# Optimization experiments

Measured on AMD Instinct MI355X. Metric: run time of the kernel, lower is better.

The kernel has to match this reference:

```python
import jax, jax.numpy as jnp
import numpy as np

N, E, IN_F, H, F = 4096, 131072, 512, 8, 32  # n_nodes, n_edges, in_features, n_heads, n_hidden
SLOPE = 0.2


def setup_inputs() -> dict:
    key = jax.random.key(0)
    k1, k2, k3, k4 = jax.random.split(key, 4)
    h = jax.random.normal(k1, (N, IN_F), dtype=jnp.float32)
    edge_index = jax.random.randint(k2, (2, E), 0, N)
    train_mask = jnp.ones((E + N,), dtype=jnp.float32)  # mask values written into adj (incl. self-loops appended in forward)
    W_fc = jax.random.normal(k3, (IN_F, H * F), dtype=jnp.float32) * (1.0 / np.sqrt(IN_F))
    W_attn = jax.random.normal(k4, (2 * F,), dtype=jnp.float32) * (1.0 / np.sqrt(2 * F))
    return {"h": h, "edge_index": edge_index, "train_mask": train_mask, "W_fc": W_fc, "W_attn": W_attn}


def reference(h, edge_index, train_mask, W_fc, W_attn):
    n = h.shape[0]
    g = (h @ W_fc).reshape(n, H, F)  # [n, H, F]
    # attn_fc(concat(g_i, g_j)) == g_i @ W_attn[:F] + g_j @ W_attn[F:]  (same math, no NxNx2F tensor)
    el = g @ W_attn[:F]  # [n, H], contribution of source row i
    er = g @ W_attn[F:]  # [n, H], contribution of column j
    e = jax.nn.leaky_relu(el[:, None, :] + er[None, :, :], SLOPE)  # [n, n, H]
    # adjacency: edges (+ self-loops appended in forward) get train_mask values, then diagonal forced to 1
    src = jnp.concatenate([edge_index[0], jnp.arange(n)])
    dst = jnp.concatenate([edge_index[1], jnp.arange(n)])
    adj = jnp.zeros((n, n), dtype=h.dtype).at[src, dst].set(train_mask)
    diag = jnp.arange(n)
    adj = adj.at[diag, diag].set(1.0)
    e = jnp.where(adj[:, :, None] == 0, -jnp.inf, e)
    a = jax.nn.softmax(e, axis=1)  # softmax over neighbors j (dropout p=0 -> identity)
    attn_res = jnp.einsum('ijh,jhf->ihf', a, g)  # [n, H, F]
    return attn_res.reshape(n, H * F)  # is_concat=True
```

## Files before the change

### kernel.cpp

```cpp
#include <hip/hip_runtime.h>
#include <stdint.h>

#define NN   4096
#define NE   131072
#define KIN  512
#define NH   8
#define HF   256
#define SLOPE 0.2f
#define MAXJ 256

typedef __attribute__((ext_vector_type(8))) short bf16x8;
typedef __attribute__((ext_vector_type(4))) float f32x4;


__device__ __forceinline__ unsigned short f2bf(float x) {
  unsigned u = __builtin_bit_cast(unsigned, x);
  u += 0x7FFFu + ((u >> 16) & 1u);
  return (unsigned short)(u >> 16);
}
__device__ __forceinline__ float bf2f(unsigned short x) {
  unsigned u = ((unsigned)x) << 16;
  return __builtin_bit_cast(float, u);
}
__device__ __forceinline__ unsigned pack2(float lo, float hi) {
  return (unsigned)f2bf(lo) | ((unsigned)f2bf(hi) << 16);
}

__global__ __launch_bounds__(256) void prep_k(const float* __restrict__ B,
                                              unsigned* __restrict__ bitmap,
                                              unsigned short* __restrict__ Btbf) {
  __shared__ float tile[32][33];
  const int b = blockIdx.x, t = threadIdx.x;
  if (b < 128) {
    float4* p = (float4*)bitmap + (size_t)b * 1024;
#pragma unroll
    for (int it = 0; it < 4; ++it)
      p[it * 256 + t] = make_float4(0.f, 0.f, 0.f, 0.f);
  } else {
    int bb = b - 128;
    int k0 = (bb >> 3) * 32, n0 = (bb & 7) * 32;
    int lr = t >> 3, lc = (t & 7) * 4;
    float4 v = *(const float4*)&B[(size_t)(k0 + lr) * HF + n0 + lc];
    tile[lr][lc] = v.x; tile[lr][lc + 1] = v.y; tile[lr][lc + 2] = v.z; tile[lr][lc + 3] = v.w;
    __syncthreads();
    ushort4 o;
    o.x = f2bf(tile[lc + 0][lr]); o.y = f2bf(tile[lc + 1][lr]);
    o.z = f2bf(tile[lc + 2][lr]); o.w = f2bf(tile[lc + 3][lr]);
    *(ushort4*)&Btbf[(size_t)(n0 + lr) * KIN + k0 + lc] = o;
  }
}

__global__ __launch_bounds__(256) void gemm_adj_k(const float* __restrict__ h,
                                                  const unsigned short* __restrict__ Bt,
                                                  const float* __restrict__ Wa,
                                                  unsigned short* __restrict__ gbf,
                                                  float* __restrict__ el,
                                                  float* __restrict__ er,
                                                  const int* __restrict__ ei,
                                                  const float* __restrict__ mask,
                                                  unsigned* __restrict__ bitmap) {
  __shared__ unsigned short smem[2][4096];
  const int bx = blockIdx.x, t = threadIdx.x;
  if (bx >= 1024) {
    int k = (bx - 1024) * 256 + t;
    int s, d; float m;
    if (k < NE) { s = ei[k]; d = ei[NE + k]; m = mask[k]; }
    else        { s = k - NE; d = s; m = 1.0f; }
    if (m != 0.0f) atomicOr(&bitmap[s * 128 + (d >> 5)], 1u << (d & 31));
    return;
  }
  const int gx = bx & 127, gy = bx >> 7;
  const int row0 = gx * 32, col0 = gy * 32;
  const int w = t >> 6, l = t & 63;
  const int wr = w >> 1, wc = w & 1;

  const int srow = (w << 3) + (l >> 3);
  const int sc   = l & 7;
  const int aoff = srow * 64 + ((sc ^ (srow & 7)) << 3);
  const float* gA = &h[(size_t)(row0 + srow) * KIN + sc * 8];
  const int schB = sc ^ (srow & 7);
  const unsigned short* gB = &Bt[(size_t)(col0 + srow) * KIN + schB * 8];

#define BSTAGE(bf, ks)                                                                            \
  __builtin_amdgcn_global_load_lds(                                                               \
      (const __attribute__((address_space(1))) unsigned int*)(gB + (size_t)(ks) * 64),            \
      (__attribute__((address_space(3))) unsigned int*)(&smem[bf][2048 + w * 512]), 16, 0, 0)

  f32x4 acc = {};
  {
    float4 va0 = *(const float4*)(gA);
    float4 va1 = *(const float4*)(gA + 4);
    BSTAGE(0, 0);
    uint4 w4 = {pack2(va0.x, va0.y), pack2(va0.z, va0.w),
                pack2(va1.x, va1.y), pack2(va1.z, va1.w)};
    *(uint4*)&smem[0][aoff] = w4;
  }
  __syncthreads();

  const int lrow = l & 15, kg = l >> 4;
  const int ar = wr * 16 + lrow, br = wc * 16 + lrow;
  for (int ks = 0; ks < 8; ++ks) {
    const int bf = ks & 1;
    float4 na0, na1;
    if (ks < 7) {
      na0 = *(const float4*)(gA + (ks + 1) * 64);
      na1 = *(const float4*)(gA + (ks + 1) * 64 + 4);
      BSTAGE(bf ^ 1, ks + 1);
    }
    bf16x8 a0 = *(const bf16x8*)&smem[bf][ar * 64 + ((kg ^ (ar & 7)) << 3)];
    bf16x8 a1 = *(const bf16x8*)&smem[bf][ar * 64 + (((4 + kg) ^ (ar & 7)) << 3)];
    bf16x8 b0 = *(const bf16x8*)&smem[bf][2048 + br * 64 + ((kg ^ (br & 7)) << 3)];
    bf16x8 b1 = *(const bf16x8*)&smem[bf][2048 + br * 64 + (((4 + kg) ^ (br & 7)) << 3)];
    acc = __builtin_amdgcn_mfma_f32_16x16x32_bf16(a0, b0, acc, 0, 0, 0);
    acc = __builtin_amdgcn_mfma_f32_16x16x32_bf16(a1, b1, acc, 0, 0, 0);
    if (ks < 7) {
      uint4 w4 = {pack2(na0.x, na0.y), pack2(na0.z, na0.w),
                  pack2(na1.x, na1.y), pack2(na1.z, na1.w)};
      *(uint4*)&smem[bf ^ 1][aoff] = w4;
    }
    __syncthreads();
  }
#undef BSTAGE

  const int crow = (l >> 4) * 4, ccol = l & 15;
  const int gr0 = row0 + wr * 16 + crow, gc = col0 + wc * 16 + ccol;
#pragma unroll
  for (int q = 0; q < 4; ++q) gbf[(size_t)(gr0 + q) * HF + gc] = f2bf(acc[q]);

  float* red = (float*)smem;
  const int f = wc * 16 + ccol;
  const float wal = Wa[f], war = Wa[32 + f];
#pragma unroll
  for (int q = 0; q < 4; ++q) {
    float pel = acc[q] * wal, per = acc[q] * war;
#pragma unroll
    for (int m = 8; m >= 1; m >>= 1) { pel += __shfl_xor(pel, m); per += __shfl_xor(per, m); }
    if (ccol == 0) {
      int rl = wr * 16 + crow + q;
      red[wc * 32 + rl] = pel;
      red[64 + wc * 32 + rl] = per;
    }
  }
  __syncthreads();
  if (t < 32) {
    el[(row0 + t) * NH + gy] = red[t] + red[32 + t];
    er[(row0 + t) * NH + gy] = red[64 + t] + red[96 + t];
  }
}

__global__ __launch_bounds__(512) void attn_k(const unsigned* __restrict__ bitmap,
                                              const unsigned short* __restrict__ gbf,
                                              const float* __restrict__ el_,
                                              const float* __restrict__ er_,
                                              float* __restrict__ out) {
  __shared__ unsigned short jl[8][MAXJ];
  const int t = threadIdx.x, wv = t >> 6, l = t & 63;
  const int i = blockIdx.x * 8 + wv;

  unsigned w0 = bitmap[i * 128 + l];
  unsigned w1 = bitmap[i * 128 + 64 + l];
  int cnt = __popc(w0) + __popc(w1);
  int incl = cnt;
#pragma unroll
  for (int d = 1; d < 64; d <<= 1) {
    int u = __shfl_up(incl, d);
    if (l >= d) incl += u;
  }
  int total = __shfl(incl, 63);
  if (total > MAXJ) total = MAXJ;
  int off = incl - cnt;
  unsigned short* J = jl[wv];
  while (w0) {
    int b = __ffs(w0) - 1;
    if (off < MAXJ) J[off] = (unsigned short)(l * 32 + b);
    ++off; w0 &= w0 - 1;
  }
  while (w1) {
    int b = __ffs(w1) - 1;
    if (off < MAXJ) J[off] = (unsigned short)((64 + l) * 32 + b);
    ++off; w1 &= w1 - 1;
  }
  __syncthreads();

  const int hh = l >> 3;
  const float elh = el_[i * NH + hh];
  const unsigned short* gp = gbf + (size_t)l * 4;
  f32x4 accA = {}, accB = {};
  float den0 = 0.f, den1 = 0.f;
  int k = 0;
  for (; k + 4 <= total; k += 4) {
    int j0 = J[k], j1 = J[k + 1], j2 = J[k + 2], j3 = J[k + 3];
    float e0 = elh + er_[j0 * NH + hh];
    float e1 = elh + er_[j1 * NH + hh];
    float e2 = elh + er_[j2 * NH + hh];
    float e3 = elh + er_[j3 * NH + hh];
    ushort4 g0 = *(const ushort4*)(gp + (size_t)j0 * HF);
    ushort4 g1 = *(const ushort4*)(gp + (size_t)j1 * HF);
    ushort4 g2 = *(const ushort4*)(gp + (size_t)j2 * HF);
    ushort4 g3 = *(const ushort4*)(gp + (size_t)j3 * HF);
    float l0 = e0 > 0.f ? e0 : SLOPE * e0;
    float l1 = e1 > 0.f ? e1 : SLOPE * e1;
    float l2 = e2 > 0.f ? e2 : SLOPE * e2;
    float l3 = e3 > 0.f ? e3 : SLOPE * e3;
    float wg0 = __expf(l0), wg1 = __expf(l1), wg2 = __expf(l2), wg3 = __expf(l3);
    den0 += wg0 + wg2; den1 += wg1 + wg3;
    accA[0] += wg0 * bf2f(g0.x); accB[0] += wg1 * bf2f(g1.x);
    accA[1] += wg0 * bf2f(g0.y); accB[1] += wg1 * bf2f(g1.y);
    accA[2] += wg0 * bf2f(g0.z); accB[2] += wg1 * bf2f(g1.z);
    accA[3] += wg0 * bf2f(g0.w); accB[3] += wg1 * bf2f(g1.w);
    accA[0] += wg2 * bf2f(g2.x); accB[0] += wg3 * bf2f(g3.x);
    accA[1] += wg2 * bf2f(g2.y); accB[1] += wg3 * bf2f(g3.y);
    accA[2] += wg2 * bf2f(g2.z); accB[2] += wg3 * bf2f(g3.z);
    accA[3] += wg2 * bf2f(g2.w); accB[3] += wg3 * bf2f(g3.w);
  }
  for (; k < total; ++k) {
    int j0 = J[k];
    float e0 = elh + er_[j0 * NH + hh];
    float l0 = e0 > 0.f ? e0 : SLOPE * e0;
    float wg0 = __expf(l0);
    ushort4 g0 = *(const ushort4*)(gp + (size_t)j0 * HF);
    den0 += wg0;
    accA[0] += wg0 * bf2f(g0.x); accA[1] += wg0 * bf2f(g0.y);
    accA[2] += wg0 * bf2f(g0.z); accA[3] += wg0 * bf2f(g0.w);
  }
  float inv = 1.f / (den0 + den1);
  float4 o = make_float4((accA[0] + accB[0]) * inv, (accA[1] + accB[1]) * inv,
                         (accA[2] + accB[2]) * inv, (accA[3] + accB[3]) * inv);
  *(float4*)&out[(size_t)i * HF + l * 4] = o;
}

extern "C" void kernel_launch(void* const* d_in, const int* in_sizes, int n_in,
                              void* d_out, int out_size, void* d_ws, size_t ws_size,
                              hipStream_t stream) {
  const float* h      = (const float*)d_in[0];
  const int*   ei     = (const int*)d_in[1];
  const float* mask   = (const float*)d_in[2];
  const float* W_fc   = (const float*)d_in[3];
  const float* W_attn = (const float*)d_in[4];
  float* out = (float*)d_out;

  char* ws = (char*)d_ws;
  unsigned* bitmap      = (unsigned*)ws;
  unsigned short* gbf   = (unsigned short*)(ws + (size_t)2 * 1024 * 1024);
  float* el             = (float*)(ws + (size_t)4 * 1024 * 1024);
  float* er             = (float*)(ws + (size_t)4 * 1024 * 1024 + 128 * 1024);
  unsigned short* Btbf  = (unsigned short*)(ws + (size_t)4 * 1024 * 1024 + 256 * 1024);

  prep_k<<<256, 256, 0, stream>>>(W_fc, bitmap, Btbf);
  gemm_adj_k<<<1024 + 528, 256, 0, stream>>>(h, Btbf, W_attn, gbf, el, er, ei, mask, bitmap);
  attn_k<<<NN / 8, 512, 0, stream>>>(bitmap, gbf, el, er, out);
}
```

Measured before the change: 33.45 us.

## Widen GEMM tile to 32x64 so each wave computes a full head

The projection GEMM now uses 32x64 output tiles instead of 32x32, halving the GEMM block count. Each wave computes two 16x16 MFMA accumulators over 32 columns, one full head, so the A tile is reused across twice as many columns. The el/er attention-logit reduction is finished within a wave by shuffles and written directly, removing the shared-memory cross-wave reduction and its barrier. The trade-off is fewer blocks (less parallelism), more LDS per block and more registers per thread.

New measurement: 33.13 us, median of 2. About the same (-1.0%).

```diff
diff --git a/kernel.cpp b/kernel.cpp
--- a/kernel.cpp
+++ b/kernel.cpp
@@ -59,10 +59,10 @@
                                                   const int* __restrict__ ei,
                                                   const float* __restrict__ mask,
                                                   unsigned* __restrict__ bitmap) {
-  __shared__ unsigned short smem[2][4096];
+  __shared__ unsigned short smem[2][6144];
   const int bx = blockIdx.x, t = threadIdx.x;
-  if (bx >= 1024) {
-    int k = (bx - 1024) * 256 + t;
+  if (bx >= 512) {
+    int k = (bx - 512) * 256 + t;
     int s, d; float m;
     if (k < NE) { s = ei[k]; d = ei[NE + k]; m = mask[k]; }
     else        { s = k - NE; d = s; m = 1.0f; }
@@ -70,23 +70,30 @@
     return;
   }
   const int gx = bx & 127, gy = bx >> 7;
-  const int row0 = gx * 32, col0 = gy * 32;
+  const int row0 = gx * 32, col0 = gy * 64;
   const int w = t >> 6, l = t & 63;
   const int wr = w >> 1, wc = w & 1;
 
-  const int srow = (w << 3) + (l >> 3);
+  const int srow = t >> 3;
   const int sc   = l & 7;
-  const int aoff = srow * 64 + ((sc ^ (srow & 7)) << 3);
-  const float* gA = &h[(size_t)(row0 + srow) * KIN + sc * 8];
-  const int schB = sc ^ (srow & 7);
-  const unsigned short* gB = &Bt[(size_t)(col0 + srow) * KIN + schB * 8];
+  const int aoff = srow * 64 + (((t & 7) ^ (srow & 7)) << 3);
+  const float* gA = &h[(size_t)(row0 + srow) * KIN + (t & 7) * 8];
+  const int bsrow = (w << 3) + (l >> 3);
+  const int schB  = sc ^ (bsrow & 7);
+  const unsigned short* gB0 = &Bt[(size_t)(col0 + bsrow) * KIN + schB * 8];
+  const unsigned short* gB1 = &Bt[(size_t)(col0 + 32 + bsrow) * KIN + schB * 8];
 
 #define BSTAGE(bf, ks)                                                                            \
-  __builtin_amdgcn_global_load_lds(                                                               \
-      (const __attribute__((address_space(1))) unsigned int*)(gB + (size_t)(ks) * 64),            \
-      (__attribute__((address_space(3))) unsigned int*)(&smem[bf][2048 + w * 512]), 16, 0, 0)
-
-  f32x4 acc = {};
+  do {                                                                                            \
+    __builtin_amdgcn_global_load_lds(                                                             \
+        (const __attribute__((address_space(1))) unsigned int*)(gB0 + (size_t)(ks) * 64),         \
+        (__attribute__((address_space(3))) unsigned int*)(&smem[bf][2048 + w * 512]), 16, 0, 0);  \
+    __builtin_amdgcn_global_load_lds(                                                             \
+        (const __attribute__((address_space(1))) unsigned int*)(gB1 + (size_t)(ks) * 64),         \
+        (__attribute__((address_space(3))) unsigned int*)(&smem[bf][4096 + w * 512]), 16, 0, 0);  \
+  } while (0)
+
+  f32x4 acc0 = {}, acc1 = {};
   {
     float4 va0 = *(const float4*)(gA);
     float4 va1 = *(const float4*)(gA + 4);
@@ -98,7 +105,8 @@
   __syncthreads();
 
   const int lrow = l & 15, kg = l >> 4;
-  const int ar = wr * 16 + lrow, br = wc * 16 + lrow;
+  const int ar  = wr * 16 + lrow;
+  const int br0 = wc * 32 + lrow, br1 = wc * 32 + 16 + lrow;
   for (int ks = 0; ks < 8; ++ks) {
     const int bf = ks & 1;
     float4 na0, na1;
@@ -109,10 +117,14 @@
     }
     bf16x8 a0 = *(const bf16x8*)&smem[bf][ar * 64 + ((kg ^ (ar & 7)) << 3)];
     bf16x8 a1 = *(const bf16x8*)&smem[bf][ar * 64 + (((4 + kg) ^ (ar & 7)) << 3)];
-    bf16x8 b0 = *(const bf16x8*)&smem[bf][2048 + br * 64 + ((kg ^ (br & 7)) << 3)];
-    bf16x8 b1 = *(const bf16x8*)&smem[bf][2048 + br * 64 + (((4 + kg) ^ (br & 7)) << 3)];
-    acc = __builtin_amdgcn_mfma_f32_16x16x32_bf16(a0, b0, acc, 0, 0, 0);
-    acc = __builtin_amdgcn_mfma_f32_16x16x32_bf16(a1, b1, acc, 0, 0, 0);
+    bf16x8 b00 = *(const bf16x8*)&smem[bf][2048 + br0 * 64 + ((kg ^ (br0 & 7)) << 3)];
+    bf16x8 b01 = *(const bf16x8*)&smem[bf][2048 + br0 * 64 + (((4 + kg) ^ (br0 & 7)) << 3)];
+    bf16x8 b10 = *(const bf16x8*)&smem[bf][2048 + br1 * 64 + ((kg ^ (br1 & 7)) << 3)];
+    bf16x8 b11 = *(const bf16x8*)&smem[bf][2048 + br1 * 64 + (((4 + kg) ^ (br1 & 7)) << 3)];
+    acc0 = __builtin_amdgcn_mfma_f32_16x16x32_bf16(a0, b00, acc0, 0, 0, 0);
+    acc0 = __builtin_amdgcn_mfma_f32_16x16x32_bf16(a1, b01, acc0, 0, 0, 0);
+    acc1 = __builtin_amdgcn_mfma_f32_16x16x32_bf16(a0, b10, acc1, 0, 0, 0);
+    acc1 = __builtin_amdgcn_mfma_f32_16x16x32_bf16(a1, b11, acc1, 0, 0, 0);
     if (ks < 7) {
       uint4 w4 = {pack2(na0.x, na0.y), pack2(na0.z, na0.w),
                   pack2(na1.x, na1.y), pack2(na1.z, na1.w)};
@@ -123,28 +135,27 @@
 #undef BSTAGE
 
   const int crow = (l >> 4) * 4, ccol = l & 15;
-  const int gr0 = row0 + wr * 16 + crow, gc = col0 + wc * 16 + ccol;
-#pragma unroll
-  for (int q = 0; q < 4; ++q) gbf[(size_t)(gr0 + q) * HF + gc] = f2bf(acc[q]);
-
-  float* red = (float*)smem;
-  const int f = wc * 16 + ccol;
-  const float wal = Wa[f], war = Wa[32 + f];
+  const int gr0 = row0 + wr * 16 + crow;
+  const int gc0 = col0 + wc * 32 + ccol, gc1 = gc0 + 16;
 #pragma unroll
   for (int q = 0; q < 4; ++q) {
-    float pel = acc[q] * wal, per = acc[q] * war;
+    gbf[(size_t)(gr0 + q) * HF + gc0] = f2bf(acc0[q]);
+    gbf[(size_t)(gr0 + q) * HF + gc1] = f2bf(acc1[q]);
+  }
+
+  const int head = (gy << 1) + wc;
+  const float wal0 = Wa[ccol],      wal1 = Wa[16 + ccol];
+  const float war0 = Wa[32 + ccol], war1 = Wa[48 + ccol];
+#pragma unroll
+  for (int q = 0; q < 4; ++q) {
+    float pel = acc0[q] * wal0 + acc1[q] * wal1;
+    float per = acc0[q] * war0 + acc1[q] * war1;
 #pragma unroll
     for (int m = 8; m >= 1; m >>= 1) { pel += __shfl_xor(pel, m); per += __shfl_xor(per, m); }
     if (ccol == 0) {
-      int rl = wr * 16 + crow + q;
-      red[wc * 32 + rl] = pel;
-      red[64 + wc * 32 + rl] = per;
+      el[(gr0 + q) * NH + head] = pel;
+      er[(gr0 + q) * NH + head] = per;
     }
-  }
-  __syncthreads();
-  if (t < 32) {
-    el[(row0 + t) * NH + gy] = red[t] + red[32 + t];
-    er[(row0 + t) * NH + gy] = red[64 + t] + red[96 + t];
   }
 }
 
@@ -247,6 +258,6 @@
   unsigned short* Btbf  = (unsigned short*)(ws + (size_t)4 * 1024 * 1024 + 256 * 1024);
 
   prep_k<<<256, 256, 0, stream>>>(W_fc, bitmap, Btbf);
-  gemm_adj_k<<<1024 + 528, 256, 0, stream>>>(h, Btbf, W_attn, gbf, el, er, ei, mask, bitmap);
+  gemm_adj_k<<<512 + 528, 256, 0, stream>>>(h, Btbf, W_attn, gbf, el, er, ei, mask, bitmap);
   attn_k<<<NN / 8, 512, 0, stream>>>(bitmap, gbf, el, er, out);
 }
```
